# Optimization experiments

Measured on AMD Instinct MI355X. Metric: run time of the kernel, lower is better.

Reference implementation:

```python
import jax, jax.numpy as jnp
import numpy as np

C = 1024      # n_feature // 2
OUT = 128     # out_dim
B, T, F = 16, 512, 2048


def conv1d(x, w, b):
    # x: [B, C, T], w: [O, I, 3], padding=1 stride=1 (torch Conv1d semantics)
    y = jax.lax.conv_general_dilated(x, w, window_strides=(1,), padding=[(1, 1)],
                                     dimension_numbers=('NCH', 'OIH', 'NCH'))
    return y + b[None, :, None]


def setup_inputs() -> dict:
    key = jax.random.key(0)
    ks = jax.random.split(key, 20)
    s = 0.02
    inp = {
        'inputs': jax.random.normal(ks[0], (B, T, F), jnp.float32),
        'wq': jax.random.normal(ks[1], (C, C, 3), jnp.float32) * s,
        'bq': jnp.zeros((C,), jnp.float32),
        'wk': jax.random.normal(ks[2], (C, C, 3), jnp.float32) * s,
        'bk': jnp.zeros((C,), jnp.float32),
        'wv': jax.random.normal(ks[3], (C, C, 3), jnp.float32) * s,
        'bv': jnp.zeros((C,), jnp.float32),
        'gamma': jax.random.normal(ks[4], (), jnp.float32) * 0.5,
        'w_fcf': jax.random.normal(ks[5], (C, C), jnp.float32) * s,
        'b_fcf': jnp.zeros((C,), jnp.float32),
        'w_fc1f': jax.random.normal(ks[6], (OUT, C), jnp.float32) * s,
        'b_fc1f': jnp.zeros((OUT,), jnp.float32),
        'w_fcr': jax.random.normal(ks[7], (C, C), jnp.float32) * s,
        'b_fcr': jnp.zeros((C,), jnp.float32),
        'w_fc1r': jax.random.normal(ks[8], (OUT, C), jnp.float32) * s,
        'b_fc1r': jnp.zeros((OUT,), jnp.float32),
        'inputs_len': jax.random.randint(ks[9], (B,), 64, T, dtype=jnp.int32),
        'is_query': 1,
    }
    return inp


def reference(inputs, wq, bq, wk, bk, wv, bv, gamma,
              w_fcf, b_fcf, w_fc1f, b_fc1f, w_fcr, b_fcr, w_fc1r, b_fc1r,
              inputs_len, is_query):
    nby2 = inputs.shape[-1] // 2
    base_x_f = inputs[:, :, nby2:]
    base_x_r = inputs[:, :, :nby2]

    def ragged_self_att(x):
        # x: [B, T, C]; attention only over each sample's first q_len frames,
        # remaining frames passed through untouched (matches per-sample slicing).
        b, t, c = x.shape
        pos = jnp.arange(t)
        mask = pos[None, :] < inputs_len[:, None]            # [B, T]
        xm = x * mask[..., None]                              # zero beyond q_len => conv zero-pad semantics at boundary
        xc = jnp.transpose(xm, (0, 2, 1))                     # [B, C, T]
        q = jnp.transpose(conv1d(xc, wq, bq), (0, 2, 1))      # [B, T, C]
        k = conv1d(xc, wk, bk)                                # [B, C, T]
        v = conv1d(xc, wv, bv)                                # [B, C, T]
        scale = jnp.sqrt(inputs_len.astype(x.dtype))[:, None, None]  # sqrt(dep)=sqrt(q_len)
        scores = jnp.einsum('btc,bcs->bts', q, k) / scale     # [B, T, T]
        scores = jnp.where(mask[:, None, :], scores, -jnp.inf)
        attn = jax.nn.softmax(scores, axis=-1)
        out = jnp.einsum('bcs,bts->btc', v, attn)             # bmm(v, attn^T), transposed to [B,T,C]
        feat = gamma * out + xm
        return jnp.where(mask[..., None], feat, x)

    a_f = ragged_self_att(base_x_f)
    a_r = ragged_self_att(base_x_r)

    def head(x, w1, b1, w2, b2):
        h = jax.nn.relu(jnp.einsum('btc,oc->bto', x, w1) + b1)
        # dropout skipped (eval / deterministic reference)
        return jax.nn.relu(jnp.einsum('btc,oc->bto', h, w2) + b2)

    y_f = head(a_f, w_fcf, b_fcf, w_fc1f, b_fc1f)
    y_r = head(a_r, w_fcr, b_fcr, w_fc1r, b_fc1r)
    return jnp.concatenate([y_f, y_r], axis=-1)              # [B, T, 2*OUT]
```

## Files before the change

### kernel.cpp

```cpp
#include <hip/hip_runtime.h>
#include <hip/hip_bf16.h>

typedef unsigned short u16;
typedef __attribute__((ext_vector_type(8))) __bf16 bf16x8;
typedef __attribute__((ext_vector_type(4))) float f32x4;

__device__ __forceinline__ u16 f2b(float f) {
  __hip_bfloat16 h = __float2bfloat16(f);
  u16 u;
  __builtin_memcpy(&u, &h, 2);
  return u;
}

__device__ __forceinline__ void gload16(const void* g, void* l) {
  __builtin_amdgcn_global_load_lds(
      (const __attribute__((address_space(1))) unsigned int*)g,
      (__attribute__((address_space(3))) unsigned int*)l, 16, 0, 0);
}

__device__ __forceinline__ bf16x8 ldsA(const char* base, int row, int ch) {
  return *(const bf16x8*)(base + row * 128 + ((ch ^ (row & 7)) << 4));
}

struct G2 {
  const u16* A;
  const u16* Bt;
  const u16* Bt2;
  void* out;
  void* out2;
  void* out3;
  const float* bias;
  const float* bias2;
  const float* bias3;
  const u16* zpage;
  int K;
};

#define STAGE_A(kt, bi)                                                        \
  {                                                                            \
    _Pragma("unroll") for (int r_ = 0; r_ < 4; ++r_) {                         \
      const int idx_ = r_ * 512 + tid;                                         \
      const int row_ = idx_ >> 3;                                              \
      const int k_ = (kt) * 64 + (((idx_ & 7) ^ (row_ & 7)) << 3);             \
      const u16* src_;                                                         \
      if constexpr (TAG == 0) {                                                \
        const int gm_ = m0 + row_;                                             \
        const int t_ = (gm_ & 511) + (k_ >> 10) - 1;                           \
        src_ = ((unsigned)t_ < 512u)                                           \
                   ? p.A + ((((long)(gm_ >> 9) << 9) + t_) << 10) + (k_ & 1023)\
                   : p.zpage;                                                  \
      } else {                                                                 \
        src_ = p.A + (long)(m0 + row_) * 1024 + k_;                            \
      }                                                                        \
      gload16(src_, (char*)lds + (bi) * 65536 + r_ * 8192 + w * 1024);         \
    }                                                                          \
  }

#define STAGE_B(kt, bi)                                                        \
  {                                                                            \
    _Pragma("unroll") for (int r_ = 0; r_ < 4; ++r_) {                         \
      const int idx_ = r_ * 512 + tid;                                         \
      const int row_ = idx_ >> 3;                                              \
      const int k_ = (kt) * 64 + (((idx_ & 7) ^ (row_ & 7)) << 3);             \
      const u16* src_ = Bb + (long)(n0 + row_) * LDB + k_;                     \
      gload16(src_, (char*)lds + (bi) * 65536 + 32768 + r_ * 8192 + w * 1024); \
    }                                                                          \
  }

#define PHASE(bi, qm, s, LOADB, STAGE_CODE)                                    \
  {                                                                            \
    const char* Ab_ = (const char*)lds + (bi) * 65536;                         \
    bf16x8 aF[4];                                                              \
    const int ch_ = (s) * 4 + (lane >> 4);                                     \
    const int r0_ = wr * 128 + (qm) * 64 + (lane & 15);                        \
    _Pragma("unroll") for (int fi = 0; fi < 4; ++fi)                           \
        aF[fi] = ldsA(Ab_, r0_ + fi * 16, ch_);                                \
    if (LOADB) {                                                               \
      const int rb_ = wc * 64 + (lane & 15);                                   \
      _Pragma("unroll") for (int ni = 0; ni < 4; ++ni)                         \
          bF[ni] = ldsA(Ab_ + 32768, rb_ + ni * 16, ch_);                      \
    }                                                                          \
    STAGE_CODE                                                                 \
    __builtin_amdgcn_s_barrier();                                              \
    __builtin_amdgcn_s_setprio(1);                                             \
    _Pragma("unroll") for (int fi = 0; fi < 4; ++fi)                           \
        _Pragma("unroll") for (int ni = 0; ni < 4; ++ni)                       \
            acc[(qm) * 4 + fi][ni] = __builtin_amdgcn_mfma_f32_16x16x32_bf16(  \
                aF[fi], bF[ni], acc[(qm) * 4 + fi][ni], 0, 0, 0);              \
    __builtin_amdgcn_s_setprio(0);                                             \
  }

template <int TAG>
__global__ __launch_bounds__(512, 2) void gemm256_k(G2 p) {
  __shared__ __align__(16) char lds[2 * 65536];

  constexpr int NTN = (TAG == 0) ? 12 : 4;
  constexpr int LDB = (TAG == 0) ? 3072 : 1024;

  const int tid = threadIdx.x;
  const int lane = tid & 63;
  const int w = tid >> 6;
  const int wr = w >> 2;
  const int wc = w & 3;

  const int cpx = gridDim.x >> 3;
  const int wg = (blockIdx.x & 7) * cpx + (blockIdx.x >> 3);
  const int n0 = (wg % NTN) * 256;
  const int m0 = (wg / NTN) * 256;

  const u16* Bb = (TAG == 1 && m0 >= 8192) ? p.Bt2 : p.Bt;

  const int NT = p.K >> 6;

  f32x4 acc[8][4] = {};
  bf16x8 bF[4];

  STAGE_A(0, 0);
  STAGE_B(0, 0);
  asm volatile("s_waitcnt vmcnt(0)" ::: "memory");
  __builtin_amdgcn_s_barrier();

  for (int t = 0; t < NT; ++t) {
    const int bi = t & 1;
    const bool pf = (t + 1 < NT);
    PHASE(bi, 0, 0, true, { if (pf) STAGE_A(t + 1, bi ^ 1); });
    __builtin_amdgcn_s_barrier();
    PHASE(bi, 1, 0, false, { if (pf) STAGE_B(t + 1, bi ^ 1); });
    __builtin_amdgcn_s_barrier();
    PHASE(bi, 0, 1, true, {});
    __builtin_amdgcn_s_barrier();
    PHASE(bi, 1, 1, false, {});
    asm volatile("s_waitcnt vmcnt(0)" ::: "memory");
    __builtin_amdgcn_s_barrier();
  }

  const int fr = (lane >> 4) * 4;
  const int fc = lane & 15;

  if constexpr (TAG == 0) {
    const int opid = n0 >> 10;
    const int nc = n0 & 1023;
    const float* bp = (opid == 0) ? p.bias : (opid == 1) ? p.bias2 : p.bias3;
    u16* qo = (u16*)p.out;
    u16* ko = (u16*)p.out2;
    u16* vo = (u16*)p.out3;
#pragma unroll
    for (int ni = 0; ni < 4; ++ni) {
      const int col = nc + wc * 64 + ni * 16 + fc;
      const float bsv = bp[col];
#pragma unroll
      for (int mi = 0; mi < 8; ++mi)
#pragma unroll
        for (int j = 0; j < 4; ++j) {
          const int grow = m0 + wr * 128 + mi * 16 + fr + j;
          const u16 v = f2b(acc[mi][ni][j] + bsv);
          if (opid == 0) qo[(long)grow * 1024 + col] = v;
          else if (opid == 1) ko[(long)grow * 1024 + col] = v;
          else vo[((long)(grow >> 9) * 1024 + col) * 512 + (grow & 511)] = v;
        }
    }
  } else {
    const float* bp = (m0 >> 13) ? p.bias2 : p.bias;
    u16* ho = (u16*)p.out;
#pragma unroll
    for (int ni = 0; ni < 4; ++ni) {
      const int col = n0 + wc * 64 + ni * 16 + fc;
      const float bsv = bp[col];
#pragma unroll
      for (int mi = 0; mi < 8; ++mi)
#pragma unroll
        for (int j = 0; j < 4; ++j) {
          const int grow = m0 + wr * 128 + mi * 16 + fr + j;
          ho[(long)grow * 1024 + col] = f2b(fmaxf(acc[mi][ni][j] + bsv, 0.f));
        }
    }
  }
}

enum { OP_SCORES = 2, OP_PV = 3, OP_HEAD2 = 5 };

struct GP {
  const u16* A;
  const u16* Bt;
  int lda, ldb, K;
  long sAz, sBz;
  void* out;
  const float* bias;
  const float* bias2;
  const float* gamma;
  const float* x_full;
  const int* lens;
};

template <int TAG>
__global__ __launch_bounds__(256, 4) void gemm_k(GP p) {
  __shared__ __align__(16) u16 As[128 * 64];
  __shared__ __align__(16) u16 Bs[128 * 64];

  const int tid = threadIdx.x;
  const int lane = tid & 63;
  const int w = tid >> 6;
  const int wr = (w >> 1) * 64;
  const int wc = (w & 1) * 64;
  const int m0 = blockIdx.y * 128;
  const int n0 = blockIdx.x * 128;
  const int z = blockIdx.z;

  const u16* Ab = p.A + (long)z * p.sAz;
  const u16* Bb = p.Bt + (long)z * p.sBz;

  const int sr = tid >> 3;
  const int scs = (((tid & 7) ^ ((tid >> 3) & 7)) << 3);

  f32x4 acc[4][4] = {};

  for (int k0 = 0; k0 < p.K; k0 += 64) {
#pragma unroll
    for (int R = 0; R < 4; ++R) {
      const int row = R * 32 + sr;
      const u16* srcA = Ab + (long)(m0 + row) * p.lda + (k0 + scs);
      gload16(srcA, (char*)As + R * 4096 + w * 1024);
      const u16* srcB = Bb + (long)(n0 + row) * p.ldb + (k0 + scs);
      gload16(srcB, (char*)Bs + R * 4096 + w * 1024);
    }
    __syncthreads();
#pragma unroll
    for (int kk = 0; kk < 64; kk += 32) {
      const int slot = (kk >> 3) + (lane >> 4);
      bf16x8 aF[4], bF[4];
#pragma unroll
      for (int mi = 0; mi < 4; ++mi) {
        const int r = wr + mi * 16 + (lane & 15);
        aF[mi] = *(const bf16x8*)(As + r * 64 + ((slot ^ (r & 7)) << 3));
      }
#pragma unroll
      for (int ni = 0; ni < 4; ++ni) {
        const int r = wc + ni * 16 + (lane & 15);
        bF[ni] = *(const bf16x8*)(Bs + r * 64 + ((slot ^ (r & 7)) << 3));
      }
#pragma unroll
      for (int mi = 0; mi < 4; ++mi)
#pragma unroll
        for (int ni = 0; ni < 4; ++ni)
          acc[mi][ni] = __builtin_amdgcn_mfma_f32_16x16x32_bf16(
              aF[mi], bF[ni], acc[mi][ni], 0, 0, 0);
    }
    __syncthreads();
  }

  const int fr = (lane >> 4) * 4;
  const int fc = lane & 15;

  if constexpr (TAG == OP_SCORES) {
    float* op = (float*)p.out + (long)z * 262144;
#pragma unroll
    for (int ni = 0; ni < 4; ++ni) {
      const int col = n0 + wc + ni * 16 + fc;
#pragma unroll
      for (int mi = 0; mi < 4; ++mi)
#pragma unroll
        for (int j = 0; j < 4; ++j) {
          const int row = m0 + wr + mi * 16 + fr + j;
          op[(long)row * 512 + col] = acc[mi][ni][j];
        }
    }
  } else if constexpr (TAG == OP_PV) {
    u16* op = (u16*)p.out;
    const int half = z >> 4, b = z & 15;
    const int len = p.lens[b];
    const float g = *p.gamma;
    const float* xb = p.x_full + ((long)b * 512) * 2048 + (half == 0 ? 1024 : 0);
#pragma unroll
    for (int ni = 0; ni < 4; ++ni) {
      const int col = n0 + wc + ni * 16 + fc;
#pragma unroll
      for (int mi = 0; mi < 4; ++mi)
#pragma unroll
        for (int j = 0; j < 4; ++j) {
          const int t = m0 + wr + mi * 16 + fr + j;
          const float xv = xb[(long)t * 2048 + col];
          const float r = (t < len) ? fmaf(g, acc[mi][ni][j], xv) : xv;
          op[((long)z * 512 + t) * 1024 + col] = f2b(r);
        }
    }
  } else {
    float* op = (float*)p.out;
    const float* bp = (z == 0) ? p.bias : p.bias2;
#pragma unroll
    for (int ni = 0; ni < 4; ++ni) {
      const int col = wc + ni * 16 + fc;
      const float bsv = bp[col];
#pragma unroll
      for (int mi = 0; mi < 4; ++mi)
#pragma unroll
        for (int j = 0; j < 4; ++j) {
          const int row = m0 + wr + mi * 16 + fr + j;
          op[(long)row * 256 + z * 128 + col] = fmaxf(acc[mi][ni][j] + bsv, 0.f);
        }
    }
  }
}

__global__ __launch_bounds__(256) void softmax_k(const float* scores, u16* attn,
                                                 const int* lens) {
  const int row = blockIdx.x * 4 + (threadIdx.x >> 6);
  const int lane = threadIdx.x & 63;
  const int len = lens[(row >> 9) & 15];
  const float inv = rsqrtf((float)len);
  const float* sr = scores + (long)row * 512;
  u16* ar = attn + (long)row * 512;
  float e[8];
  float mx = -1e30f;
#pragma unroll
  for (int j = 0; j < 8; ++j) {
    const int s = j * 64 + lane;
    const float v = (s < len) ? sr[s] * inv : -1e30f;
    e[j] = v;
    mx = fmaxf(mx, v);
  }
#pragma unroll
  for (int d = 1; d < 64; d <<= 1) mx = fmaxf(mx, __shfl_xor(mx, d));
  float sum = 0.f;
#pragma unroll
  for (int j = 0; j < 8; ++j) {
    const int s = j * 64 + lane;
    const float t = (s < len) ? __expf(e[j] - mx) : 0.f;
    e[j] = t;
    sum += t;
  }
#pragma unroll
  for (int d = 1; d < 64; d <<= 1) sum += __shfl_xor(sum, d);
  const float r = 1.f / sum;
#pragma unroll
  for (int j = 0; j < 8; ++j) ar[j * 64 + lane] = f2b(e[j] * r);
}

__global__ void convw_k(const float* wsrc, u16* wt) {
  const int idx = blockIdx.x * 256 + threadIdx.x;
  const float* s = wsrc + (long)idx * 3;
  u16* d = wt + (long)(idx >> 10) * 3072 + (idx & 1023);
  d[0] = f2b(s[0]);
  d[1024] = f2b(s[1]);
  d[2048] = f2b(s[2]);
}

__global__ void castk(const float* s, u16* d, int n) {
  const int i = blockIdx.x * 256 + threadIdx.x;
  if (i < n) d[i] = f2b(s[i]);
}

__global__ void xmk(const float* inputs, u16* xm, const int* lens) {
  const int idx = blockIdx.x * 256 + threadIdx.x;
  const int row = idx >> 8;
  const int c4 = (idx & 255) * 4;
  const int xoff = (row & 8192) ? 0 : 1024;
  const bool live = (row & 511) < lens[(row >> 9) & 15];
  float4 v = {0.f, 0.f, 0.f, 0.f};
  if (live) v = *(const float4*)(inputs + (long)(row & 8191) * 2048 + xoff + c4);
  ushort4 o;
  o.x = f2b(v.x); o.y = f2b(v.y); o.z = f2b(v.z); o.w = f2b(v.w);
  *(ushort4*)(xm + (long)row * 1024 + c4) = o;
}

__global__ void zerok(u16* p) { p[blockIdx.x * 256 + threadIdx.x] = 0; }

extern "C" void kernel_launch(void* const* d_in, const int* in_sizes, int n_in,
                              void* d_out, int out_size, void* d_ws, size_t ws_size,
                              hipStream_t stream) {
  const float* inputs = (const float*)d_in[0];
  const float* wq = (const float*)d_in[1];
  const float* bq = (const float*)d_in[2];
  const float* wk = (const float*)d_in[3];
  const float* bk = (const float*)d_in[4];
  const float* wv = (const float*)d_in[5];
  const float* bv = (const float*)d_in[6];
  const float* gamma = (const float*)d_in[7];
  const float* w_fcf = (const float*)d_in[8];
  const float* b_fcf = (const float*)d_in[9];
  const float* w_fc1f = (const float*)d_in[10];
  const float* b_fc1f = (const float*)d_in[11];
  const float* w_fcr = (const float*)d_in[12];
  const float* b_fcr = (const float*)d_in[13];
  const float* w_fc1r = (const float*)d_in[14];
  const float* b_fc1r = (const float*)d_in[15];
  const int* lens = (const int*)d_in[16];
  float* out = (float*)d_out;

  char* ws = (char*)d_ws;
  size_t off = 0;
  auto alloc = [&](size_t n) {
    char* p = ws + off;
    off += (n + 255) & ~(size_t)255;
    return p;
  };

  u16* wt_all = (u16*)alloc(3072l * 3072 * 2);
  u16* zpage = (u16*)alloc(4096);
  u16* xm = (u16*)alloc(16384l * 1024 * 2);
  u16* qb = (u16*)alloc(16384l * 1024 * 2);
  u16* kb = (u16*)alloc(16384l * 1024 * 2);
  u16* vb = (u16*)alloc(32l * 1024 * 512 * 2);
  u16* attn = wt_all;
  float* scores = (float*)xm;
  u16* w1b = (u16*)xm;
  u16* w2b = w1b + 2l * 1024 * 1024;
  u16* abuf = qb;
  u16* hbuf = kb;

  zerok<<<8, 256, 0, stream>>>(zpage);
  convw_k<<<4096, 256, 0, stream>>>(wq, wt_all);
  convw_k<<<4096, 256, 0, stream>>>(wk, wt_all + 1024l * 3072);
  convw_k<<<4096, 256, 0, stream>>>(wv, wt_all + 2048l * 3072);
  xmk<<<16384, 256, 0, stream>>>(inputs, xm, lens);

  {
    G2 g{};
    g.A = xm; g.Bt = wt_all; g.zpage = zpage; g.K = 3072;
    g.out = qb; g.out2 = kb; g.out3 = vb;
    g.bias = bq; g.bias2 = bk; g.bias3 = bv;
    gemm256_k<0><<<768, 512, 0, stream>>>(g);
  }

  {
    GP g{};
    g.A = qb; g.Bt = kb; g.lda = 1024; g.ldb = 1024; g.K = 1024;
    g.sAz = 512l * 1024; g.sBz = 512l * 1024; g.out = scores;
    gemm_k<OP_SCORES><<<dim3(4, 4, 32), 256, 0, stream>>>(g);
  }
  softmax_k<<<4096, 256, 0, stream>>>(scores, attn, lens);

  castk<<<4096, 256, 0, stream>>>(w_fcf, w1b, 1024 * 1024);
  castk<<<4096, 256, 0, stream>>>(w_fcr, w1b + 1024l * 1024, 1024 * 1024);
  castk<<<512, 256, 0, stream>>>(w_fc1f, w2b, 128 * 1024);
  castk<<<512, 256, 0, stream>>>(w_fc1r, w2b + 128l * 1024, 128 * 1024);

  {
    GP g{};
    g.A = attn; g.Bt = vb; g.lda = 512; g.ldb = 512; g.K = 512;
    g.sAz = 512l * 512; g.sBz = 1024l * 512;
    g.out = abuf; g.gamma = gamma; g.x_full = inputs; g.lens = lens;
    gemm_k<OP_PV><<<dim3(8, 4, 32), 256, 0, stream>>>(g);
  }

  {
    G2 h{};
    h.A = abuf; h.Bt = w1b; h.Bt2 = w1b + 1024l * 1024; h.K = 1024;
    h.out = hbuf; h.bias = b_fcf; h.bias2 = b_fcr;
    gemm256_k<1><<<256, 512, 0, stream>>>(h);
  }

  {
    GP g{};
    g.A = hbuf; g.Bt = w2b; g.lda = 1024; g.ldb = 1024; g.K = 1024;
    g.sAz = 8192l * 1024; g.sBz = 128l * 1024;
    g.out = out; g.bias = b_fc1f; g.bias2 = b_fc1r;
    gemm_k<OP_HEAD2><<<dim3(1, 64, 2), 256, 0, stream>>>(g);
  }
}
```

Before: 694.7 us.

## Switch GEMM to 4-stage BK=32 pipeline with 3-tile prefetch

Restructures the main bf16 GEMM loop from a double-buffered BK=64 scheme with four sub-phases and many barriers to a four-buffer ring of BK=32 tiles. Three tiles are prefetched ahead, and each iteration needs one waitcnt and one barrier. The LDS swizzle is adapted to 64-byte rows. The goal is deeper overlap of global-to-LDS loads with MFMA work and less barrier overhead. In exchange, each iteration does less compute, and the kernel now holds 8 A-fragment registers at once, which raises register pressure.

```diff
diff --git a/kernel.cpp b/kernel.cpp
--- a/kernel.cpp
+++ b/kernel.cpp
@@ -18,8 +18,8 @@
       (__attribute__((address_space(3))) unsigned int*)l, 16, 0, 0);
 }
 
-__device__ __forceinline__ bf16x8 ldsA(const char* base, int row, int ch) {
-  return *(const bf16x8*)(base + row * 128 + ((ch ^ (row & 7)) << 4));
+__device__ __forceinline__ bf16x8 ldsF(const char* base, int row, int ch) {
+  return *(const bf16x8*)(base + row * 64 + ((ch ^ ((row >> 1) & 3)) << 4));
 }
 
 struct G2 {
@@ -36,12 +36,12 @@
   int K;
 };
 
-#define STAGE_A(kt, bi)                                                        \
+#define STG(kt, bi)                                                            \
   {                                                                            \
-    _Pragma("unroll") for (int r_ = 0; r_ < 4; ++r_) {                         \
+    _Pragma("unroll") for (int r_ = 0; r_ < 2; ++r_) {                         \
       const int idx_ = r_ * 512 + tid;                                         \
-      const int row_ = idx_ >> 3;                                              \
-      const int k_ = (kt) * 64 + (((idx_ & 7) ^ (row_ & 7)) << 3);             \
+      const int row_ = idx_ >> 2;                                              \
+      const int k_ = (kt) * 32 + (((idx_ & 3) ^ ((row_ >> 1) & 3)) << 3);      \
       const u16* src_;                                                         \
       if constexpr (TAG == 0) {                                                \
         const int gm_ = m0 + row_;                                             \
@@ -52,47 +52,39 @@
       } else {                                                                 \
         src_ = p.A + (long)(m0 + row_) * 1024 + k_;                            \
       }                                                                        \
-      gload16(src_, (char*)lds + (bi) * 65536 + r_ * 8192 + w * 1024);         \
+      gload16(src_, (char*)lds + (bi) * 32768 + r_ * 8192 + w * 1024);         \
     }                                                                          \
-  }
-
-#define STAGE_B(kt, bi)                                                        \
+    _Pragma("unroll") for (int r_ = 0; r_ < 2; ++r_) {                         \
+      const int idx_ = r_ * 512 + tid;                                         \
+      const int row_ = idx_ >> 2;                                              \
+      const int k_ = (kt) * 32 + (((idx_ & 3) ^ ((row_ >> 1) & 3)) << 3);      \
+      const u16* src_ = Bb + (long)(n0 + row_) * LDB + k_;                     \
+      gload16(src_, (char*)lds + (bi) * 32768 + 16384 + r_ * 8192 + w * 1024); \
+    }                                                                          \
+  }
+
+#define CMP(bi)                                                                \
   {                                                                            \
-    _Pragma("unroll") for (int r_ = 0; r_ < 4; ++r_) {                         \
-      const int idx_ = r_ * 512 + tid;                                         \
-      const int row_ = idx_ >> 3;                                              \
-      const int k_ = (kt) * 64 + (((idx_ & 7) ^ (row_ & 7)) << 3);             \
-      const u16* src_ = Bb + (long)(n0 + row_) * LDB + k_;                     \
-      gload16(src_, (char*)lds + (bi) * 65536 + 32768 + r_ * 8192 + w * 1024); \
-    }                                                                          \
-  }
-
-#define PHASE(bi, qm, s, LOADB, STAGE_CODE)                                    \
-  {                                                                            \
-    const char* Ab_ = (const char*)lds + (bi) * 65536;                         \
-    bf16x8 aF[4];                                                              \
-    const int ch_ = (s) * 4 + (lane >> 4);                                     \
-    const int r0_ = wr * 128 + (qm) * 64 + (lane & 15);                        \
-    _Pragma("unroll") for (int fi = 0; fi < 4; ++fi)                           \
-        aF[fi] = ldsA(Ab_, r0_ + fi * 16, ch_);                                \
-    if (LOADB) {                                                               \
-      const int rb_ = wc * 64 + (lane & 15);                                   \
-      _Pragma("unroll") for (int ni = 0; ni < 4; ++ni)                         \
-          bF[ni] = ldsA(Ab_ + 32768, rb_ + ni * 16, ch_);                      \
-    }                                                                          \
-    STAGE_CODE                                                                 \
-    __builtin_amdgcn_s_barrier();                                              \
+    const char* Ab_ = (const char*)lds + (bi) * 32768;                         \
+    bf16x8 aF[8], bF[4];                                                       \
+    const int ch_ = lane >> 4;                                                 \
+    const int rA_ = wr * 128 + (lane & 15);                                    \
+    const int rB_ = wc * 64 + (lane & 15);                                     \
+    _Pragma("unroll") for (int mi = 0; mi < 8; ++mi)                           \
+        aF[mi] = ldsF(Ab_, rA_ + mi * 16, ch_);                                \
+    _Pragma("unroll") for (int ni = 0; ni < 4; ++ni)                           \
+        bF[ni] = ldsF(Ab_ + 16384, rB_ + ni * 16, ch_);                        \
     __builtin_amdgcn_s_setprio(1);                                             \
-    _Pragma("unroll") for (int fi = 0; fi < 4; ++fi)                           \
+    _Pragma("unroll") for (int mi = 0; mi < 8; ++mi)                           \
         _Pragma("unroll") for (int ni = 0; ni < 4; ++ni)                       \
-            acc[(qm) * 4 + fi][ni] = __builtin_amdgcn_mfma_f32_16x16x32_bf16(  \
-                aF[fi], bF[ni], acc[(qm) * 4 + fi][ni], 0, 0, 0);              \
+            acc[mi][ni] = __builtin_amdgcn_mfma_f32_16x16x32_bf16(             \
+                aF[mi], bF[ni], acc[mi][ni], 0, 0, 0);                         \
     __builtin_amdgcn_s_setprio(0);                                             \
   }
 
 template <int TAG>
 __global__ __launch_bounds__(512, 2) void gemm256_k(G2 p) {
-  __shared__ __align__(16) char lds[2 * 65536];
+  __shared__ __align__(16) char lds[4 * 32768];
 
   constexpr int NTN = (TAG == 0) ? 12 : 4;
   constexpr int LDB = (TAG == 0) ? 3072 : 1024;
@@ -110,29 +102,32 @@
 
   const u16* Bb = (TAG == 1 && m0 >= 8192) ? p.Bt2 : p.Bt;
 
-  const int NT = p.K >> 6;
+  const int NT = p.K >> 5;
 
   f32x4 acc[8][4] = {};
-  bf16x8 bF[4];
-
-  STAGE_A(0, 0);
-  STAGE_B(0, 0);
+
+  STG(0, 0);
+  STG(1, 1);
+  STG(2, 2);
+  asm volatile("s_waitcnt vmcnt(8)" ::: "memory");
+  __builtin_amdgcn_s_barrier();
+
+  int t = 0;
+  for (; t < NT - 3; ++t) {
+    STG(t + 3, (t + 3) & 3);
+    CMP(t & 3);
+    asm volatile("s_waitcnt vmcnt(8)" ::: "memory");
+    __builtin_amdgcn_s_barrier();
+  }
+  CMP(t & 3);
+  asm volatile("s_waitcnt vmcnt(4)" ::: "memory");
+  __builtin_amdgcn_s_barrier();
+  ++t;
+  CMP(t & 3);
   asm volatile("s_waitcnt vmcnt(0)" ::: "memory");
   __builtin_amdgcn_s_barrier();
-
-  for (int t = 0; t < NT; ++t) {
-    const int bi = t & 1;
-    const bool pf = (t + 1 < NT);
-    PHASE(bi, 0, 0, true, { if (pf) STAGE_A(t + 1, bi ^ 1); });
-    __builtin_amdgcn_s_barrier();
-    PHASE(bi, 1, 0, false, { if (pf) STAGE_B(t + 1, bi ^ 1); });
-    __builtin_amdgcn_s_barrier();
-    PHASE(bi, 0, 1, true, {});
-    __builtin_amdgcn_s_barrier();
-    PHASE(bi, 1, 1, false, {});
-    asm volatile("s_waitcnt vmcnt(0)" ::: "memory");
-    __builtin_amdgcn_s_barrier();
-  }
+  ++t;
+  CMP(t & 3);
 
   const int fr = (lane >> 4) * 4;
   const int fc = lane & 15;
```

New measurement: 678.5 us. -2.3%, faster.
